# Performance work log

Hardware: AMD Instinct MI355X
Metric: run time of the kernel (lower is better)

## Reference

```python
import jax, jax.numpy as jnp
import numpy as np

NEG_INF = -1e9  # finite large-negative for the additive causal mask
N, H, S, SKV, K, V = 4, 16, 2048, 2048, 128, 128


def setup_inputs() -> dict:
    key = jax.random.key(0)
    k1, k2, k3, k4 = jax.random.split(key, 4)
    seqs = jax.random.normal(k1, (N, H, S, K), dtype=jnp.float32)
    keys = jax.random.normal(k2, (N, H, SKV, K), dtype=jnp.float32)
    values = jax.random.normal(k3, (N, H, SKV, V), dtype=jnp.float32)
    # boolean keep-mask; force first key position valid so no row is fully masked
    kpm = jax.random.randint(k4, (N, SKV), 0, 2) > 0
    kpm = kpm.at[:, 0].set(True)
    # causal additive attention mask, shape (S, S_kv)
    causal = jnp.tril(jnp.ones((S, SKV), dtype=bool))
    attn_mask = jnp.where(causal, 0.0, NEG_INF).astype(jnp.float32)
    return {"seqs": seqs, "keys": keys, "values": values,
            "key_padding_mask": kpm, "attn_mask": attn_mask}


def reference(seqs, keys, values, key_padding_mask, attn_mask):
    # attn_weights: [N,H,S,S_kv]
    scale = seqs.shape[-1] ** -0.5
    w = jnp.einsum('bhsk,bhtk->bhst', seqs, keys) * scale
    w = w + attn_mask  # broadcast (S,S_kv) over (N,H)
    w = jnp.where(key_padding_mask[:, None, None, :], w, -jnp.inf)
    # softmax computed in fp32, then cast back to input dtype (matches torch)
    p = jax.nn.softmax(w.astype(jnp.float32), axis=-1).astype(seqs.dtype)
    attn = jnp.einsum('bhst,bhtv->bhsv', p, values)
    return attn
```

## Files before the change

kernel.cpp:

```cpp
#include <hip/hip_runtime.h>

#define S_Q 2048
#define S_KV 2048
#define D_K 128
#define NH 64
#define NB 4
#define QSCALE 0.12751494907890272f

typedef __attribute__((ext_vector_type(8))) short s16x8;
typedef __attribute__((ext_vector_type(16))) float f32x16;

__device__ __attribute__((aligned(16))) unsigned short g_Kb[(size_t)NH * S_KV * D_K];
__device__ __attribute__((aligned(16))) unsigned short g_Vt[(size_t)NH * D_K * S_KV];
__device__ __attribute__((aligned(16))) unsigned short g_kpmf[NB * S_KV];

__device__ inline unsigned short f2bf(float f) {
  unsigned int u = __float_as_uint(f);
  u += 0x7FFFu + ((u >> 16) & 1u);
  return (unsigned short)(u >> 16);
}

__device__ inline unsigned cvt_pk_bf16(float lo, float hi) {
  unsigned r;
  asm("v_cvt_pk_bf16_f32 %0, %1, %2" : "=v"(r) : "v"(lo), "v"(hi));
  return r;
}

__device__ inline void plane32_swap(unsigned& a, unsigned& b) {
#if __has_builtin(__builtin_amdgcn_permlane32_swap)
  typedef unsigned __attribute__((ext_vector_type(2))) u32x2;
  u32x2 r = __builtin_amdgcn_permlane32_swap(a, b, false, false);
  a = r.x; b = r.y;
#else
  asm volatile("v_permlane32_swap_b32 %0, %1" : "+v"(a), "+v"(b));
#endif
}

__global__ __launch_bounds__(256) void prep_k_kernel(const float* __restrict__ K,
                                                     const int* __restrict__ kpm) {
  size_t g = (size_t)blockIdx.x * 256 + threadIdx.x;
  const float* src = K + g * 8;
  float4 x = *(const float4*)src;
  float4 y = *(const float4*)(src + 4);
  union { uint4 q; unsigned short u[8]; } t;
  t.u[0] = f2bf(x.x); t.u[1] = f2bf(x.y); t.u[2] = f2bf(x.z); t.u[3] = f2bf(x.w);
  t.u[4] = f2bf(y.x); t.u[5] = f2bf(y.y); t.u[6] = f2bf(y.z); t.u[7] = f2bf(y.w);
  ((uint4*)g_Kb)[g] = t.q;
  if (g < (size_t)NB * S_KV)
    g_kpmf[g] = kpm[g] ? (unsigned short)0x3F80 : (unsigned short)0;
}

__global__ __launch_bounds__(256) void prep_v_kernel(const float* __restrict__ V,
                                                     const int* __restrict__ kpm) {
  __shared__ float tile_f[64][33];
  int bid = blockIdx.x;
  int bh = bid >> 7;
  int rem = bid & 127;
  int t0 = (rem >> 2) << 6;
  int v0 = (rem & 3) << 5;
  int c = threadIdx.x & 31;
  int r8 = threadIdx.x >> 5;
  const int* kp = kpm + (bh >> 4) * S_KV + t0;
#pragma unroll
  for (int i = 0; i < 8; i++) {
    int r = r8 + i * 8;
    float f = V[((size_t)(bh * S_KV + t0 + r)) * D_K + v0 + c];
    tile_f[r][c] = kp[r] ? f : 0.0f;
  }
  __syncthreads();
  int vv = threadIdx.x >> 3;
  int jc = threadIdx.x & 7;
  union { uint4 q; unsigned short u[8]; } t;
#pragma unroll
  for (int u8 = 0; u8 < 8; u8++) t.u[u8] = f2bf(tile_f[jc * 8 + u8][vv]);
  *(uint4*)&g_Vt[((size_t)(bh * D_K + v0 + vv)) * S_KV + t0 + jc * 8] = t.q;
}

__global__ __launch_bounds__(256, 3) void attn_kernel(const float* __restrict__ Q,
                                                      float* __restrict__ out) {
  __shared__ __attribute__((aligned(16))) unsigned short sK[2][32 * 136];
  __shared__ __attribute__((aligned(16))) unsigned short sV[2][128 * 40];
  __shared__ __attribute__((aligned(16))) unsigned short sLall[S_KV];

  const int bx = blockIdx.x;
  const int bh = ((bx & 7) << 3) | ((bx >> 3) & 7);
  int qp = bx >> 6;
  int qi = (qp & 4) ? ((qp & 8) ? qp - 8 : qp - 4) : ((qp & 8) ? 19 - qp : 15 - qp);
  const int q0 = qi << 7;
  const int tid = threadIdx.x;
  const int w = tid >> 6;
  const int ln = tid & 31;
  const int h = (tid >> 5) & 1;
  const int h8 = h * 8;
  const int qw = q0 + w * 32;
  const int qln = qw + ln;
  const int b = bh >> 4;
  const unsigned short* gkpm = g_kpmf + (size_t)b * S_KV;

  s16x8 qf[8];
  {
    const float* qrow = Q + ((size_t)(bh * S_Q + qln)) * D_K + h8;
#pragma unroll
    for (int kc = 0; kc < 8; kc++) {
      float4 x = *(const float4*)(qrow + kc * 16);
      float4 y = *(const float4*)(qrow + kc * 16 + 4);
      union { s16x8 v; unsigned short u[8]; } t;
      t.u[0] = f2bf(x.x * QSCALE); t.u[1] = f2bf(x.y * QSCALE);
      t.u[2] = f2bf(x.z * QSCALE); t.u[3] = f2bf(x.w * QSCALE);
      t.u[4] = f2bf(y.x * QSCALE); t.u[5] = f2bf(y.y * QSCALE);
      t.u[6] = f2bf(y.z * QSCALE); t.u[7] = f2bf(y.w * QSCALE);
      qf[kc] = t.v;
    }
  }

  const int id0 = tid, id1 = 256 + tid;
  const int kr0r = id0 >> 4, kr0c = (id0 & 15) * 8;
  const int kr1r = id1 >> 4, kr1c = (id1 & 15) * 8;
  const int vr0r = id0 >> 2, vr0c = (id0 & 3) * 8;
  const int vr1r = id1 >> 2, vr1c = (id1 & 3) * 8;
  uint4 rk0, rk1, rv0, rv1;
  auto load_tile = [&](int t0) {
    rk0 = *(const uint4*)&g_Kb[((size_t)(bh * S_KV + t0 + kr0r)) * D_K + kr0c];
    rk1 = *(const uint4*)&g_Kb[((size_t)(bh * S_KV + t0 + kr1r)) * D_K + kr1c];
    rv0 = *(const uint4*)&g_Vt[((size_t)(bh * D_K + vr0r)) * S_KV + t0 + vr0c];
    rv1 = *(const uint4*)&g_Vt[((size_t)(bh * D_K + vr1r)) * S_KV + t0 + vr1c];
  };
  auto store_tile = [&](int buf) {
    *(uint4*)&sK[buf][kr0r * 136 + kr0c] = rk0;
    *(uint4*)&sK[buf][kr1r * 136 + kr1c] = rk1;
    *(uint4*)&sV[buf][vr0r * 40 + vr0c] = rv0;
    *(uint4*)&sV[buf][vr1r * 40 + vr1c] = rv1;
  };

  f32x16 o[4] = {f32x16{}, f32x16{}, f32x16{}, f32x16{}};
  f32x16 lacc = {};

  const int nT = qi * 4 + 4;
  load_tile(0);
  store_tile(0);
  *(uint4*)&sLall[tid * 8] = *(const uint4*)(gkpm + tid * 8);
  load_tile(32);
  __syncthreads();

  for (int i = 0; i < nT; i++) {
    const int cur = i & 1;
    if (i + 1 < nT) {
      store_tile(1 - cur);
      if (i + 2 < nT) load_tile((i + 2) * 32);
    }
    const int t0 = i * 32;
    if (t0 <= qw) {
      f32x16 sa = {};
#pragma unroll
      for (int kc = 0; kc < 8; kc++) {
        s16x8 kb = *(const s16x8*)&sK[cur][ln * 136 + kc * 16 + h8];
        sa = __builtin_amdgcn_mfma_f32_32x32x16_bf16(kb, qf[kc], sa, 0, 0, 0);
      }
      float p[16];
#pragma unroll
      for (int r = 0; r < 16; r++) p[r] = __builtin_amdgcn_exp2f(sa[r]);
      if (t0 == qw) {
#pragma unroll
        for (int r = 0; r < 16; r++) {
          int tl = (r & 3) + 8 * (r >> 2) + 4 * h;
          if (tl > ln) p[r] = 0.0f;
        }
      }
      unsigned d[8];
#pragma unroll
      for (int m = 0; m < 4; m++) {
        d[2 * m] = cvt_pk_bf16(p[4 * m + 0], p[4 * m + 1]);
        d[2 * m + 1] = cvt_pk_bf16(p[4 * m + 2], p[4 * m + 3]);
      }
      plane32_swap(d[0], d[2]); plane32_swap(d[1], d[3]);
      plane32_swap(d[4], d[6]); plane32_swap(d[5], d[7]);
      union { unsigned u[4]; s16x8 v; } pu0, pu1;
      pu0.u[0] = d[0]; pu0.u[1] = d[1]; pu0.u[2] = d[2]; pu0.u[3] = d[3];
      pu1.u[0] = d[4]; pu1.u[1] = d[5]; pu1.u[2] = d[6]; pu1.u[3] = d[7];
      s16x8 lva0 = *(const s16x8*)&sLall[i * 32 + h8];
      s16x8 lva1 = *(const s16x8*)&sLall[i * 32 + 16 + h8];
#pragma unroll
      for (int vt = 0; vt < 4; vt++) {
        s16x8 va = *(const s16x8*)&sV[cur][(vt * 32 + ln) * 40 + h8];
        s16x8 vb = *(const s16x8*)&sV[cur][(vt * 32 + ln) * 40 + 16 + h8];
        o[vt] = __builtin_amdgcn_mfma_f32_32x32x16_bf16(va, pu0.v, o[vt], 0, 0, 0);
        o[vt] = __builtin_amdgcn_mfma_f32_32x32x16_bf16(vb, pu1.v, o[vt], 0, 0, 0);
      }
      lacc = __builtin_amdgcn_mfma_f32_32x32x16_bf16(lva0, pu0.v, lacc, 0, 0, 0);
      lacc = __builtin_amdgcn_mfma_f32_32x32x16_bf16(lva1, pu1.v, lacc, 0, 0, 0);
    }
    __builtin_amdgcn_sched_barrier(0);
    asm volatile("s_waitcnt lgkmcnt(0)" ::: "memory");
    __builtin_amdgcn_s_barrier();
    __builtin_amdgcn_sched_barrier(0);
  }

  float invl = 1.0f / lacc[0];
  size_t orow = ((size_t)(bh * S_Q + qln)) * D_K;
#pragma unroll
  for (int vt = 0; vt < 4; vt++) {
#pragma unroll
    for (int qd = 0; qd < 4; qd++) {
      float4 vv;
      vv.x = o[vt][4 * qd + 0] * invl;
      vv.y = o[vt][4 * qd + 1] * invl;
      vv.z = o[vt][4 * qd + 2] * invl;
      vv.w = o[vt][4 * qd + 3] * invl;
      *(float4*)&out[orow + vt * 32 + qd * 8 + 4 * h] = vv;
    }
  }
}

extern "C" void kernel_launch(void* const* d_in, const int* in_sizes, int n_in,
                              void* d_out, int out_size, void* d_ws, size_t ws_size,
                              hipStream_t stream) {
  const float* Q = (const float*)d_in[0];
  const float* K = (const float*)d_in[1];
  const float* V = (const float*)d_in[2];
  const int* kpm = (const int*)d_in[3];
  float* out = (float*)d_out;
  hipLaunchKernelGGL(prep_k_kernel, dim3(8192), dim3(256), 0, stream, K, kpm);
  hipLaunchKernelGGL(prep_v_kernel, dim3(8192), dim3(256), 0, stream, V, kpm);
  hipLaunchKernelGGL(attn_kernel, dim3(1024), dim3(256), 0, stream, Q, out);
}
```

Measured before the change: 362.0 us.

## Stream K/V tiles via global_load_lds with XOR-swizzled LDS and merge prep kernels

New measurement: 321.3 us. 11.2% less time.

```diff
diff --git a/kernel.cpp b/kernel.cpp
--- a/kernel.cpp
+++ b/kernel.cpp
@@ -36,51 +36,57 @@
 #endif
 }
 
-__global__ __launch_bounds__(256) void prep_k_kernel(const float* __restrict__ K,
-                                                     const int* __restrict__ kpm) {
-  size_t g = (size_t)blockIdx.x * 256 + threadIdx.x;
-  const float* src = K + g * 8;
-  float4 x = *(const float4*)src;
-  float4 y = *(const float4*)(src + 4);
-  union { uint4 q; unsigned short u[8]; } t;
-  t.u[0] = f2bf(x.x); t.u[1] = f2bf(x.y); t.u[2] = f2bf(x.z); t.u[3] = f2bf(x.w);
-  t.u[4] = f2bf(y.x); t.u[5] = f2bf(y.y); t.u[6] = f2bf(y.z); t.u[7] = f2bf(y.w);
-  ((uint4*)g_Kb)[g] = t.q;
-  if (g < (size_t)NB * S_KV)
-    g_kpmf[g] = kpm[g] ? (unsigned short)0x3F80 : (unsigned short)0;
-}
-
-__global__ __launch_bounds__(256) void prep_v_kernel(const float* __restrict__ V,
-                                                     const int* __restrict__ kpm) {
+__device__ inline void gload_lds16(const void* g, void* l) {
+  __builtin_amdgcn_global_load_lds((const __attribute__((address_space(1))) void*)g,
+                                   (__attribute__((address_space(3))) void*)l, 16, 0, 0);
+}
+
+__global__ __launch_bounds__(256) void prep_kernel(const float* __restrict__ K,
+                                                   const float* __restrict__ V,
+                                                   const int* __restrict__ kpm) {
   __shared__ float tile_f[64][33];
-  int bid = blockIdx.x;
-  int bh = bid >> 7;
-  int rem = bid & 127;
-  int t0 = (rem >> 2) << 6;
-  int v0 = (rem & 3) << 5;
-  int c = threadIdx.x & 31;
-  int r8 = threadIdx.x >> 5;
-  const int* kp = kpm + (bh >> 4) * S_KV + t0;
-#pragma unroll
-  for (int i = 0; i < 8; i++) {
-    int r = r8 + i * 8;
-    float f = V[((size_t)(bh * S_KV + t0 + r)) * D_K + v0 + c];
-    tile_f[r][c] = kp[r] ? f : 0.0f;
-  }
-  __syncthreads();
-  int vv = threadIdx.x >> 3;
-  int jc = threadIdx.x & 7;
-  union { uint4 q; unsigned short u[8]; } t;
-#pragma unroll
-  for (int u8 = 0; u8 < 8; u8++) t.u[u8] = f2bf(tile_f[jc * 8 + u8][vv]);
-  *(uint4*)&g_Vt[((size_t)(bh * D_K + v0 + vv)) * S_KV + t0 + jc * 8] = t.q;
+  const int bid = blockIdx.x;
+  if (bid < 8192) {
+    size_t g = (size_t)bid * 256 + threadIdx.x;
+    const float* src = K + g * 8;
+    float4 x = *(const float4*)src;
+    float4 y = *(const float4*)(src + 4);
+    union { uint4 q; unsigned short u[8]; } t;
+    t.u[0] = f2bf(x.x); t.u[1] = f2bf(x.y); t.u[2] = f2bf(x.z); t.u[3] = f2bf(x.w);
+    t.u[4] = f2bf(y.x); t.u[5] = f2bf(y.y); t.u[6] = f2bf(y.z); t.u[7] = f2bf(y.w);
+    ((uint4*)g_Kb)[g] = t.q;
+    if (g < (size_t)NB * S_KV)
+      g_kpmf[g] = kpm[g] ? (unsigned short)0x3F80 : (unsigned short)0;
+  } else {
+    const int vb = bid - 8192;
+    int bh = vb >> 7;
+    int rem = vb & 127;
+    int t0 = (rem >> 2) << 6;
+    int v0 = (rem & 3) << 5;
+    int c = threadIdx.x & 31;
+    int r8 = threadIdx.x >> 5;
+    const int* kp = kpm + (bh >> 4) * S_KV + t0;
+#pragma unroll
+    for (int i = 0; i < 8; i++) {
+      int r = r8 + i * 8;
+      float f = V[((size_t)(bh * S_KV + t0 + r)) * D_K + v0 + c];
+      tile_f[r][c] = kp[r] ? f : 0.0f;
+    }
+    __syncthreads();
+    int vv = threadIdx.x >> 3;
+    int jc = threadIdx.x & 7;
+    union { uint4 q; unsigned short u[8]; } t;
+#pragma unroll
+    for (int u8 = 0; u8 < 8; u8++) t.u[u8] = f2bf(tile_f[jc * 8 + u8][vv]);
+    *(uint4*)&g_Vt[((size_t)(bh * D_K + v0 + vv)) * S_KV + t0 + jc * 8] = t.q;
+  }
 }
 
 __global__ __launch_bounds__(256, 3) void attn_kernel(const float* __restrict__ Q,
                                                       float* __restrict__ out) {
-  __shared__ __attribute__((aligned(16))) unsigned short sK[2][32 * 136];
-  __shared__ __attribute__((aligned(16))) unsigned short sV[2][128 * 40];
-  __shared__ __attribute__((aligned(16))) unsigned short sLall[S_KV];
+  __shared__ __attribute__((aligned(16))) unsigned short sK[2][32 * 128];
+  __shared__ __attribute__((aligned(16))) unsigned short sV[2][128 * 32];
+  __shared__ __attribute__((aligned(16))) unsigned short sL[S_KV];
 
   const int bx = blockIdx.x;
   const int bh = ((bx & 7) << 3) | ((bx >> 3) & 7);
@@ -89,13 +95,13 @@
   const int q0 = qi << 7;
   const int tid = threadIdx.x;
   const int w = tid >> 6;
+  const int ln64 = tid & 63;
   const int ln = tid & 31;
   const int h = (tid >> 5) & 1;
   const int h8 = h * 8;
   const int qw = q0 + w * 32;
   const int qln = qw + ln;
   const int b = bh >> 4;
-  const unsigned short* gkpm = g_kpmf + (size_t)b * S_KV;
 
   s16x8 qf[8];
   {
@@ -113,86 +119,88 @@
     }
   }
 
-  const int id0 = tid, id1 = 256 + tid;
-  const int kr0r = id0 >> 4, kr0c = (id0 & 15) * 8;
-  const int kr1r = id1 >> 4, kr1c = (id1 & 15) * 8;
-  const int vr0r = id0 >> 2, vr0c = (id0 & 3) * 8;
-  const int vr1r = id1 >> 2, vr1c = (id1 & 3) * 8;
-  uint4 rk0, rk1, rv0, rv1;
-  auto load_tile = [&](int t0) {
-    rk0 = *(const uint4*)&g_Kb[((size_t)(bh * S_KV + t0 + kr0r)) * D_K + kr0c];
-    rk1 = *(const uint4*)&g_Kb[((size_t)(bh * S_KV + t0 + kr1r)) * D_K + kr1c];
-    rv0 = *(const uint4*)&g_Vt[((size_t)(bh * D_K + vr0r)) * S_KV + t0 + vr0c];
-    rv1 = *(const uint4*)&g_Vt[((size_t)(bh * D_K + vr1r)) * S_KV + t0 + vr1c];
+  int srcK[2], srcV[2];
+#pragma unroll
+  for (int r = 0; r < 2; r++) {
+    const int L = r * 4096 + w * 1024 + ln64 * 16;
+    const int t = L >> 8, c = L & 255;
+    srcK[r] = t * 256 + (c ^ ((t & 7) << 4));
+    const int m = L >> 7, p = L & 127;
+    const int a = ((p >> 6) ^ (m >> 1)) & 1;
+    const int tb = ((((p >> 5) ^ m) & 1) << 5) | ((((p >> 4) ^ a) & 1) << 4) | (p & 15);
+    srcV[r] = (2 * m + a) * (S_KV * 2) + tb;
+  }
+  const char* gK = (const char*)g_Kb + (size_t)bh * (S_KV * D_K * 2);
+  const char* gV = (const char*)g_Vt + (size_t)bh * (D_K * S_KV * 2);
+  auto dma_tile = [&](int buf, int tt) {
+    const char* kb = gK + tt * 256;
+    const char* vb = gV + tt * 2;
+    gload_lds16(kb + srcK[0], &sK[buf][w * 512]);
+    gload_lds16(kb + srcK[1], &sK[buf][w * 512 + 2048]);
+    gload_lds16(vb + srcV[0], &sV[buf][w * 512]);
+    gload_lds16(vb + srcV[1], &sV[buf][w * 512 + 2048]);
   };
-  auto store_tile = [&](int buf) {
-    *(uint4*)&sK[buf][kr0r * 136 + kr0c] = rk0;
-    *(uint4*)&sK[buf][kr1r * 136 + kr1c] = rk1;
-    *(uint4*)&sV[buf][vr0r * 40 + vr0c] = rv0;
-    *(uint4*)&sV[buf][vr1r * 40 + vr1c] = rv1;
-  };
+
+  const int kb_base = ln * 256 + ((h << 4) ^ ((ln & 7) << 4));
+  const int vb0 = (ln >> 1) * 128 + ((((ln & 1) << 6) | (h << 4)) ^ ((ln & 7) << 4));
+  const int vb1 = vb0 ^ 32;
 
   f32x16 o[4] = {f32x16{}, f32x16{}, f32x16{}, f32x16{}};
   f32x16 lacc = {};
 
   const int nT = qi * 4 + 4;
-  load_tile(0);
-  store_tile(0);
-  *(uint4*)&sLall[tid * 8] = *(const uint4*)(gkpm + tid * 8);
-  load_tile(32);
+  dma_tile(0, 0);
+  *(uint4*)&sL[tid * 8] = *(const uint4*)(g_kpmf + (size_t)b * S_KV + tid * 8);
   __syncthreads();
 
   for (int i = 0; i < nT; i++) {
     const int cur = i & 1;
-    if (i + 1 < nT) {
-      store_tile(1 - cur);
-      if (i + 2 < nT) load_tile((i + 2) * 32);
-    }
+    if (i + 1 < nT) dma_tile(1 - cur, (i + 1) * 32);
     const int t0 = i * 32;
     if (t0 <= qw) {
+      const char* sKc = (const char*)&sK[cur][0];
+      const char* sVc = (const char*)&sV[cur][0];
       f32x16 sa = {};
 #pragma unroll
       for (int kc = 0; kc < 8; kc++) {
-        s16x8 kb = *(const s16x8*)&sK[cur][ln * 136 + kc * 16 + h8];
-        sa = __builtin_amdgcn_mfma_f32_32x32x16_bf16(kb, qf[kc], sa, 0, 0, 0);
-      }
-      float p[16];
-#pragma unroll
-      for (int r = 0; r < 16; r++) p[r] = __builtin_amdgcn_exp2f(sa[r]);
+        s16x8 kbf = *(const s16x8*)(sKc + (kb_base ^ (kc * 32)));
+        sa = __builtin_amdgcn_mfma_f32_32x32x16_bf16(kbf, qf[kc], sa, 0, 0, 0);
+      }
       if (t0 == qw) {
 #pragma unroll
         for (int r = 0; r < 16; r++) {
           int tl = (r & 3) + 8 * (r >> 2) + 4 * h;
-          if (tl > ln) p[r] = 0.0f;
+          if (tl > ln) sa[r] = -1e30f;
         }
       }
       unsigned d[8];
 #pragma unroll
       for (int m = 0; m < 4; m++) {
-        d[2 * m] = cvt_pk_bf16(p[4 * m + 0], p[4 * m + 1]);
-        d[2 * m + 1] = cvt_pk_bf16(p[4 * m + 2], p[4 * m + 3]);
+        d[2 * m] = cvt_pk_bf16(__builtin_amdgcn_exp2f(sa[4 * m + 0]),
+                               __builtin_amdgcn_exp2f(sa[4 * m + 1]));
+        d[2 * m + 1] = cvt_pk_bf16(__builtin_amdgcn_exp2f(sa[4 * m + 2]),
+                                   __builtin_amdgcn_exp2f(sa[4 * m + 3]));
       }
       plane32_swap(d[0], d[2]); plane32_swap(d[1], d[3]);
       plane32_swap(d[4], d[6]); plane32_swap(d[5], d[7]);
       union { unsigned u[4]; s16x8 v; } pu0, pu1;
       pu0.u[0] = d[0]; pu0.u[1] = d[1]; pu0.u[2] = d[2]; pu0.u[3] = d[3];
       pu1.u[0] = d[4]; pu1.u[1] = d[5]; pu1.u[2] = d[6]; pu1.u[3] = d[7];
-      s16x8 lva0 = *(const s16x8*)&sLall[i * 32 + h8];
-      s16x8 lva1 = *(const s16x8*)&sLall[i * 32 + 16 + h8];
+      s16x8 lva0 = *(const s16x8*)((const char*)sL + i * 64 + h * 16);
+      s16x8 lva1 = *(const s16x8*)((const char*)sL + i * 64 + 32 + h * 16);
 #pragma unroll
       for (int vt = 0; vt < 4; vt++) {
-        s16x8 va = *(const s16x8*)&sV[cur][(vt * 32 + ln) * 40 + h8];
-        s16x8 vb = *(const s16x8*)&sV[cur][(vt * 32 + ln) * 40 + 16 + h8];
+        s16x8 va = *(const s16x8*)(sVc + vt * 2048 + vb0);
+        s16x8 vbf = *(const s16x8*)(sVc + vt * 2048 + vb1);
         o[vt] = __builtin_amdgcn_mfma_f32_32x32x16_bf16(va, pu0.v, o[vt], 0, 0, 0);
-        o[vt] = __builtin_amdgcn_mfma_f32_32x32x16_bf16(vb, pu1.v, o[vt], 0, 0, 0);
+        o[vt] = __builtin_amdgcn_mfma_f32_32x32x16_bf16(vbf, pu1.v, o[vt], 0, 0, 0);
       }
       lacc = __builtin_amdgcn_mfma_f32_32x32x16_bf16(lva0, pu0.v, lacc, 0, 0, 0);
       lacc = __builtin_amdgcn_mfma_f32_32x32x16_bf16(lva1, pu1.v, lacc, 0, 0, 0);
     }
     __builtin_amdgcn_sched_barrier(0);
-    asm volatile("s_waitcnt lgkmcnt(0)" ::: "memory");
+    asm volatile("s_waitcnt vmcnt(0) lgkmcnt(0)" ::: "memory");
     __builtin_amdgcn_s_barrier();
-    __builtin_amdgcn_sched_barrier(0);
   }
 
   float invl = 1.0f / lacc[0];
@@ -219,7 +227,6 @@
   const float* V = (const float*)d_in[2];
   const int* kpm = (const int*)d_in[3];
   float* out = (float*)d_out;
-  hipLaunchKernelGGL(prep_k_kernel, dim3(8192), dim3(256), 0, stream, K, kpm);
-  hipLaunchKernelGGL(prep_v_kernel, dim3(8192), dim3(256), 0, stream, V, kpm);
+  hipLaunchKernelGGL(prep_kernel, dim3(16384), dim3(256), 0, stream, K, V, kpm);
   hipLaunchKernelGGL(attn_kernel, dim3(1024), dim3(256), 0, stream, Q, out);
 }
```
